# Performance work log

Measured on AMD Instinct MI355X. Metric: run time of the kernel, lower is better.

Reference implementation:

```python
import jax, jax.numpy as jnp
import numpy as np

B, C_IN, C_OUT, L = 16, 512, 512, 2048
HEADS, K, U, KS, PAD = 4, 16, 1, 3, 1
VV = C_OUT // HEADS  # 128
EPS = 1e-5


def _conv1d(x, w, pad):
    # x: [B, Cin, L], w: [Cout, Cin, KS] -> [B, Cout, L]
    return jax.lax.conv_general_dilated(
        x, w, window_strides=(1,), padding=[(pad, pad)],
        dimension_numbers=('NCH', 'OIH', 'NCH'))


def _bn_eval(y, gamma, beta, mean, var):
    # inference-mode BatchNorm1d over channel axis
    scale = gamma * jax.lax.rsqrt(var + EPS)
    shift = beta - mean * scale
    return y * scale[None, :, None] + shift[None, :, None]


def setup_inputs() -> dict:
    key = jax.random.key(0)
    ks = jax.random.split(key, 8)
    std_q = 1.0 / np.sqrt(C_IN * KS)
    x = jax.random.normal(ks[0], (B, C_IN, L), dtype=jnp.float32)
    Wq = jax.random.normal(ks[1], (K * HEADS, C_IN, KS), dtype=jnp.float32) * std_q
    Wk = jax.random.normal(ks[2], (K * U, C_IN, KS), dtype=jnp.float32) * std_q
    Wv = jax.random.normal(ks[3], (VV * U, C_IN, KS), dtype=jnp.float32) * std_q
    embedding = jax.random.normal(ks[4], (K, U), dtype=jnp.float32)
    return {
        'x': x, 'Wq': Wq,
        'q_gamma': jnp.ones((K * HEADS,), jnp.float32),
        'q_beta': jnp.zeros((K * HEADS,), jnp.float32),
        'q_mean': jnp.zeros((K * HEADS,), jnp.float32),
        'q_var': jnp.ones((K * HEADS,), jnp.float32),
        'Wk': Wk, 'Wv': Wv,
        'v_gamma': jnp.ones((VV * U,), jnp.float32),
        'v_beta': jnp.zeros((VV * U,), jnp.float32),
        'v_mean': jnp.zeros((VV * U,), jnp.float32),
        'v_var': jnp.ones((VV * U,), jnp.float32),
        'embedding': embedding,
    }


def reference(x, Wq, q_gamma, q_beta, q_mean, q_var, Wk, Wv,
              v_gamma, v_beta, v_mean, v_var, embedding):
    batch, _, n = x.shape
    # projections
    q = _bn_eval(_conv1d(x, Wq, PAD), q_gamma, q_beta, q_mean, q_var)
    q = q.reshape(batch, HEADS, K, n)                      # bhkn
    keys = _conv1d(x, Wk, PAD).reshape(batch, K, U, n)     # bkun
    sm = jax.nn.softmax(keys, axis=-1)                     # softmax over positions
    v = _bn_eval(_conv1d(x, Wv, PAD), v_gamma, v_beta, v_mean, v_var)
    v = v.reshape(batch, VV, U, n)                         # bvun
    # content lambda
    lambda_c = jnp.einsum('bkun,bvun->bkv', sm, v)
    y_c = jnp.einsum('bhkn,bkv->bhvn', q, lambda_c)
    # position lambda
    lambda_p = jnp.einsum('ku,bvun->bkvn', embedding, v)
    y_p = jnp.einsum('bhkn,bkvn->bhvn', q, lambda_p)
    out = y_c + y_p
    return out.reshape(batch, HEADS * VV, n)
```

## Files before the change

kernel.cpp:

```cpp
#include <hip/hip_runtime.h>

#define BB 16
#define CIN 512
#define LLN 2048
#define EPSV 1e-5f

typedef __attribute__((ext_vector_type(8))) short bf16x8s;
typedef __attribute__((ext_vector_type(4))) float f32x4;

__device__ __forceinline__ unsigned short f2bf(float f) {
    union { float f; unsigned int i; } c; c.f = f;
    unsigned int x = c.i;
    unsigned int lsb = (x >> 16) & 1;
    x += 0x7fff + lsb;
    return (unsigned short)(x >> 16);
}
__device__ __forceinline__ unsigned int pack2bf(float a, float b) {
    return (unsigned int)f2bf(a) | ((unsigned int)f2bf(b) << 16);
}

__device__ __forceinline__ void g2l16(const void* g, void* l) {
    typedef const __attribute__((address_space(1))) unsigned int GU;
    typedef __attribute__((address_space(3))) unsigned int LU;
    __builtin_amdgcn_global_load_lds((GU*)g, (LU*)l, 16, 0, 0);
}

#define WIMG_U16 6144

__global__ __launch_bounds__(256) void prep_all(
    const float* __restrict__ x,
    const float* __restrict__ Wq, const float* __restrict__ Wk,
    const float* __restrict__ Wv,
    unsigned short* __restrict__ xpk, unsigned short* __restrict__ Wpk)
{
    const int tid = threadIdx.x;
    if (blockIdx.z < 16) {
        const int nt = blockIdx.x;
        const int c  = blockIdx.y;
        const int b  = blockIdx.z;
        const int n = nt * 256 + tid;
        const int rp = n + 1;
        const float* xb = x + ((size_t)b * CIN + (size_t)c * 32) * LLN + n;
        unsigned int row[16];
#pragma unroll
        for (int p = 0; p < 16; p++)
            row[p] = pack2bf(xb[(size_t)(2 * p) * LLN], xb[(size_t)(2 * p + 1) * LLN]);
        unsigned short* dst = xpk + ((size_t)(b * 16 + c) * 2050 + rp) * 32;
        const int sig = (rp >> 1) & 3;
#pragma unroll
        for (int s = 0; s < 4; s++) {
            int g = (s ^ sig) * 4;
            *(uint4*)(dst + s * 8) = make_uint4(row[g], row[g + 1], row[g + 2], row[g + 3]);
        }
        if (nt == 0 && tid < 4)
            *(uint4*)(xpk + ((size_t)(b * 16 + c) * 2050) * 32 + tid * 8) = make_uint4(0, 0, 0, 0);
        if (nt == 7 && tid < 4)
            *(uint4*)(xpk + ((size_t)(b * 16 + c) * 2050 + 2049) * 32 + tid * 8) = make_uint4(0, 0, 0, 0);
    } else {
        const int wblk = blockIdx.y * 8 + blockIdx.x;
        const int img = wblk >> 1, half = wblk & 1;
        const int cot = img >> 4, chunk = img & 15;
        const int ci0 = chunk * 32;
        for (int i = half * 3072 + tid; i < half * 3072 + 3072; i += 256) {
            int t = i >> 11, r = i & 2047;
            int cf = r >> 9, lane = (r >> 3) & 63, e = i & 7;
            int lm = lane & 15, kq = lane >> 4;
            int cop = cot * 64 + cf * 16 + lm;
            int cig = ci0 + kq * 8 + e;
            float val = 0.f;
            if (cop < 64)        val = Wq[((size_t)cop * 512 + cig) * 3 + t];
            else if (cop < 80)   val = Wk[((size_t)(cop - 64) * 512 + cig) * 3 + t];
            else if (cop < 208)  val = Wv[((size_t)(cop - 80) * 512 + cig) * 3 + t];
            Wpk[(size_t)img * WIMG_U16 + i] = f2bf(val);
        }
    }
}

__global__ __launch_bounds__(256) void conv_mfma(
    const unsigned short* __restrict__ xpk, const unsigned short* __restrict__ Wpk,
    const float* __restrict__ qg, const float* __restrict__ qb,
    const float* __restrict__ qm, const float* __restrict__ qv,
    const float* __restrict__ vg, const float* __restrict__ vb,
    const float* __restrict__ vm, const float* __restrict__ vvar,
    float* __restrict__ qbuf, float* __restrict__ kbuf, float* __restrict__ vbuf)
{
    __shared__ __align__(16) unsigned short xT[2][258 * 32];
    __shared__ __align__(16) unsigned short wA[2][WIMG_U16];
    __shared__ float sscale[64], sshift[64];

    const int tid = threadIdx.x;
    const int wave = tid >> 6, lane = tid & 63;
    const int kq = lane >> 4, lm = lane & 15;
    const int n0 = blockIdx.x * 256;
    const int cot = blockIdx.y;
    const int b = blockIdx.z;

    const unsigned short* xpanel = xpk + ((size_t)b * 16 * 2050 + n0) * 32;
    const unsigned short* wbase  = Wpk + (size_t)cot * 16 * WIMG_U16;

#define STAGE(buf, chunk)                                                      \
    {                                                                          \
        const unsigned short* wsrc = wbase + (size_t)(chunk) * WIMG_U16;       \
        const unsigned short* xsrc = xpanel + (size_t)(chunk) * 2050 * 32;     \
        for (int i = tid; i < 768; i += 256)  g2l16(wsrc + i * 8, &wA[buf][i * 8]); \
        for (int i = tid; i < 1032; i += 256) g2l16(xsrc + i * 8, &xT[buf][i * 8]); \
    }

    STAGE(0, 0)

    if (tid < 64) {
        int cop = cot * 64 + tid;
        float sc = 1.f, sh = 0.f;
        if (cop < 64) {
            float g = qg[cop], be = qb[cop], m = qm[cop], va = qv[cop];
            sc = g * rsqrtf(va + EPSV); sh = be - m * sc;
        } else if (cop >= 80 && cop < 208) {
            int cc = cop - 80;
            float g = vg[cc], be = vb[cc], m = vm[cc], va = vvar[cc];
            sc = g * rsqrtf(va + EPSV); sh = be - m * sc;
        }
        sscale[tid] = sc; sshift[tid] = sh;
    }

    f32x4 acc[4][4];
#pragma unroll
    for (int i = 0; i < 4; i++)
#pragma unroll
        for (int j = 0; j < 4; j++) acc[i][j] = (f32x4){0.f, 0.f, 0.f, 0.f};

    asm volatile("s_waitcnt vmcnt(0)" ::: "memory");
    __syncthreads();

    for (int chunk = 0; chunk < 16; chunk++) {
        const int cur = chunk & 1;
        if (chunk < 15) STAGE(cur ^ 1, chunk + 1)

#pragma unroll
        for (int t = 0; t < 3; t++) {
            bf16x8s aF[4];
#pragma unroll
            for (int cf = 0; cf < 4; cf++)
                aF[cf] = *(const bf16x8s*)&wA[cur][((t * 4 + cf) * 64 + lane) * 8];
#pragma unroll
            for (int fn = 0; fn < 4; fn++) {
                int lr = wave * 64 + fn * 16 + lm + t;
                int grp = kq ^ ((lr >> 1) & 3);
                bf16x8s bF = *(const bf16x8s*)&xT[cur][lr * 32 + grp * 8];
#pragma unroll
                for (int cf = 0; cf < 4; cf++)
                    acc[cf][fn] = __builtin_amdgcn_mfma_f32_16x16x32_bf16(
                        aF[cf], bF, acc[cf][fn], 0, 0, 0);
            }
        }
        asm volatile("s_waitcnt vmcnt(0)" ::: "memory");
        __syncthreads();
    }
#undef STAGE

#pragma unroll
    for (int cf = 0; cf < 4; cf++) {
#pragma unroll
        for (int fn = 0; fn < 4; fn++) {
#pragma unroll
            for (int r = 0; r < 4; r++) {
                int col = cf * 16 + kq * 4 + r;
                int cop = cot * 64 + col;
                if (cop >= 208) continue;
                float val = acc[cf][fn][r] * sscale[col] + sshift[col];
                int nout = n0 + wave * 64 + fn * 16 + lm;
                if (cop < 64)
                    qbuf[((size_t)b * 64 + cop) * LLN + nout] = val;
                else if (cop < 80)
                    kbuf[((size_t)b * 16 + (cop - 64)) * LLN + nout] = val;
                else
                    vbuf[((size_t)b * 128 + (cop - 80)) * LLN + nout] = val;
            }
        }
    }
}

__global__ __launch_bounds__(256) void lambdac_kernel(
    const float* __restrict__ kb, const float* __restrict__ vbuf,
    float* __restrict__ lcb)
{
    const int wave = threadIdx.x >> 6;
    const int lane = threadIdx.x & 63;
    const int b = blockIdx.x >> 5;
    const int vg = blockIdx.x & 31;
    const float* ps = kb + ((size_t)b * 16 + wave * 4) * LLN;
    const float* pv = vbuf + ((size_t)b * 128 + vg * 4) * LLN;

    float m[4] = {-1e30f, -1e30f, -1e30f, -1e30f};
#pragma unroll
    for (int j = 0; j < 8; j++) {
        int n = (j * 64 + lane) * 4;
#pragma unroll
        for (int k = 0; k < 4; k++) {
            float4 s4 = *(const float4*)&ps[(size_t)k * LLN + n];
            m[k] = fmaxf(m[k], fmaxf(fmaxf(s4.x, s4.y), fmaxf(s4.z, s4.w)));
        }
    }
#pragma unroll
    for (int k = 0; k < 4; k++)
#pragma unroll
        for (int off = 32; off > 0; off >>= 1)
            m[k] = fmaxf(m[k], __shfl_xor(m[k], off, 64));

    float sum[4] = {0.f, 0.f, 0.f, 0.f};
    float acc[4][4];
#pragma unroll
    for (int k = 0; k < 4; k++)
#pragma unroll
        for (int v = 0; v < 4; v++) acc[k][v] = 0.f;
#pragma unroll
    for (int j = 0; j < 8; j++) {
        int n = (j * 64 + lane) * 4;
        float4 e4[4];
#pragma unroll
        for (int k = 0; k < 4; k++) {
            float4 s4 = *(const float4*)&ps[(size_t)k * LLN + n];
            e4[k].x = __expf(s4.x - m[k]);
            e4[k].y = __expf(s4.y - m[k]);
            e4[k].z = __expf(s4.z - m[k]);
            e4[k].w = __expf(s4.w - m[k]);
            sum[k] += e4[k].x + e4[k].y + e4[k].z + e4[k].w;
        }
#pragma unroll
        for (int v = 0; v < 4; v++) {
            float4 v4 = *(const float4*)&pv[(size_t)v * LLN + n];
#pragma unroll
            for (int k = 0; k < 4; k++)
                acc[k][v] += e4[k].x * v4.x + e4[k].y * v4.y
                           + e4[k].z * v4.z + e4[k].w * v4.w;
        }
    }
#pragma unroll
    for (int k = 0; k < 4; k++) {
#pragma unroll
        for (int off = 32; off > 0; off >>= 1)
            sum[k] += __shfl_xor(sum[k], off, 64);
#pragma unroll
        for (int v = 0; v < 4; v++)
#pragma unroll
            for (int off = 32; off > 0; off >>= 1)
                acc[k][v] += __shfl_xor(acc[k][v], off, 64);
    }
    if (lane == 0) {
#pragma unroll
        for (int k = 0; k < 4; k++) {
            float inv = 1.f / sum[k];
#pragma unroll
            for (int v = 0; v < 4; v++)
                lcb[((size_t)b * 16 + wave * 4 + k) * 128 + vg * 4 + v] = acc[k][v] * inv;
        }
    }
}

__global__ __launch_bounds__(256) void final_kernel(
    const float* __restrict__ qbuf, const float* __restrict__ vbuf,
    const float* __restrict__ lcb, const float* __restrict__ emb,
    float* __restrict__ out)
{
    __shared__ float lcsT[128][16];
    __shared__ float es[16];
    const int tid = threadIdx.x;
    const int h = tid >> 6, nl = tid & 63;
    const int n0 = blockIdx.x * 64;
    const int b = blockIdx.y;

    for (int i = tid; i < 2048; i += 256)
        lcsT[i >> 4][i & 15] = lcb[(size_t)b * 2048 + (size_t)(i & 15) * 128 + (i >> 4)];
    if (tid < 16) es[tid] = emb[tid];
    __syncthreads();

    const int n = n0 + nl;
    const float* pq = qbuf + ((size_t)b * 64 + h * 16) * LLN + n;
    float4 q4[4];
#pragma unroll
    for (int kk = 0; kk < 4; kk++) {
        q4[kk].x = pq[(size_t)(kk * 4 + 0) * LLN];
        q4[kk].y = pq[(size_t)(kk * 4 + 1) * LLN];
        q4[kk].z = pq[(size_t)(kk * 4 + 2) * LLN];
        q4[kk].w = pq[(size_t)(kk * 4 + 3) * LLN];
    }
    float s = 0.f;
#pragma unroll
    for (int kk = 0; kk < 4; kk++)
        s += q4[kk].x * es[kk * 4] + q4[kk].y * es[kk * 4 + 1]
           + q4[kk].z * es[kk * 4 + 2] + q4[kk].w * es[kk * 4 + 3];

    const float* pv = vbuf + (size_t)b * 128 * LLN + n;
    float* po = out + ((size_t)b * 512 + h * 128) * LLN + n;
    for (int v = 0; v < 128; v++) {
        float4 c0 = *(const float4*)&lcsT[v][0];
        float4 c1 = *(const float4*)&lcsT[v][4];
        float4 c2 = *(const float4*)&lcsT[v][8];
        float4 c3 = *(const float4*)&lcsT[v][12];
        float lam = q4[0].x * c0.x + q4[0].y * c0.y + q4[0].z * c0.z + q4[0].w * c0.w
                  + q4[1].x * c1.x + q4[1].y * c1.y + q4[1].z * c1.z + q4[1].w * c1.w
                  + q4[2].x * c2.x + q4[2].y * c2.y + q4[2].z * c2.z + q4[2].w * c2.w
                  + q4[3].x * c3.x + q4[3].y * c3.y + q4[3].z * c3.z + q4[3].w * c3.w;
        float vvv = pv[(size_t)v * LLN];
        po[(size_t)v * LLN] = lam + s * vvv;
    }
}

extern "C" void kernel_launch(void* const* d_in, const int* in_sizes, int n_in,
                              void* d_out, int out_size, void* d_ws, size_t ws_size,
                              hipStream_t stream)
{
    const float* x   = (const float*)d_in[0];
    const float* Wq  = (const float*)d_in[1];
    const float* qg  = (const float*)d_in[2];
    const float* qb  = (const float*)d_in[3];
    const float* qm  = (const float*)d_in[4];
    const float* qv  = (const float*)d_in[5];
    const float* Wk  = (const float*)d_in[6];
    const float* Wv  = (const float*)d_in[7];
    const float* vg  = (const float*)d_in[8];
    const float* vb  = (const float*)d_in[9];
    const float* vm  = (const float*)d_in[10];
    const float* vva = (const float*)d_in[11];
    const float* emb = (const float*)d_in[12];
    float* out = (float*)d_out;

    float* qbuf = (float*)d_ws;
    float* kbuf = qbuf + (size_t)BB * 64 * LLN;
    float* vbuf = kbuf + (size_t)BB * 16 * LLN;
    float* lcb  = vbuf + (size_t)BB * 128 * LLN;
    unsigned short* Wpk = (unsigned short*)(lcb + (size_t)BB * 16 * 128);
    unsigned short* xpk = Wpk + (size_t)64 * WIMG_U16;

    hipLaunchKernelGGL(prep_all, dim3(8, 16, 17), dim3(256), 0, stream,
                       x, Wq, Wk, Wv, xpk, Wpk);

    hipLaunchKernelGGL(conv_mfma, dim3(8, 4, 16), dim3(256), 0, stream,
                       xpk, Wpk, qg, qb, qm, qv, vg, vb, vm, vva,
                       qbuf, kbuf, vbuf);

    hipLaunchKernelGGL(lambdac_kernel, dim3(512), dim3(256), 0, stream,
                       kbuf, vbuf, lcb);

    hipLaunchKernelGGL(final_kernel, dim3(32, BB), dim3(256), 0, stream,
                       qbuf, vbuf, lcb, emb, out);
}
```

Baseline: 204.2 us.

## Store q and v intermediates as bf16 and vectorize x packing

The conv kernel now writes q and v projections as bf16 instead of fp32, and the lambda and final kernels read and widen them, halving intermediate memory traffic. The lambda kernel is reworked to process 8 positions per lane with 16-byte bf16 loads. The x prep kernel now has each thread load float4s and pack 4 positions, using 4x fewer blocks, and the weight prep gives each block two full images. This adds bf16 rounding error to q and v before the final products.

```diff
diff --git a/kernel.cpp b/kernel.cpp
--- a/kernel.cpp
+++ b/kernel.cpp
@@ -18,6 +18,15 @@
 __device__ __forceinline__ unsigned int pack2bf(float a, float b) {
     return (unsigned int)f2bf(a) | ((unsigned int)f2bf(b) << 16);
 }
+__device__ __forceinline__ float bf2f(unsigned short u) {
+    union { unsigned int i; float f; } c; c.i = ((unsigned int)u) << 16; return c.f;
+}
+__device__ __forceinline__ float bflo(unsigned int w) {
+    union { unsigned int i; float f; } c; c.i = w << 16; return c.f;
+}
+__device__ __forceinline__ float bfhi(unsigned int w) {
+    union { unsigned int i; float f; } c; c.i = w & 0xffff0000u; return c.f;
+}
 
 __device__ __forceinline__ void g2l16(const void* g, void* l) {
     typedef const __attribute__((address_space(1))) unsigned int GU;
@@ -38,40 +47,53 @@
         const int nt = blockIdx.x;
         const int c  = blockIdx.y;
         const int b  = blockIdx.z;
-        const int n = nt * 256 + tid;
-        const int rp = n + 1;
+        const int n = nt * 1024 + tid * 4;
         const float* xb = x + ((size_t)b * CIN + (size_t)c * 32) * LLN + n;
-        unsigned int row[16];
-#pragma unroll
-        for (int p = 0; p < 16; p++)
-            row[p] = pack2bf(xb[(size_t)(2 * p) * LLN], xb[(size_t)(2 * p + 1) * LLN]);
-        unsigned short* dst = xpk + ((size_t)(b * 16 + c) * 2050 + rp) * 32;
-        const int sig = (rp >> 1) & 3;
-#pragma unroll
-        for (int s = 0; s < 4; s++) {
-            int g = (s ^ sig) * 4;
-            *(uint4*)(dst + s * 8) = make_uint4(row[g], row[g + 1], row[g + 2], row[g + 3]);
+        unsigned short* dstbase = xpk + ((size_t)(b * 16 + c) * 2050 + (n + 1)) * 32;
+#pragma unroll
+        for (int g = 0; g < 4; g++) {
+            float4 r[8];
+#pragma unroll
+            for (int q = 0; q < 8; q++)
+                r[q] = *(const float4*)&xb[(size_t)(g * 8 + q) * LLN];
+#pragma unroll
+            for (int dn = 0; dn < 4; dn++) {
+                const float* rr[8] = {(const float*)&r[0], (const float*)&r[1],
+                                      (const float*)&r[2], (const float*)&r[3],
+                                      (const float*)&r[4], (const float*)&r[5],
+                                      (const float*)&r[6], (const float*)&r[7]};
+                uint4 w = make_uint4(pack2bf(rr[0][dn], rr[1][dn]),
+                                     pack2bf(rr[2][dn], rr[3][dn]),
+                                     pack2bf(rr[4][dn], rr[5][dn]),
+                                     pack2bf(rr[6][dn], rr[7][dn]));
+                int rp = n + dn + 1;
+                int sp = g ^ ((rp >> 1) & 3);
+                *(uint4*)(dstbase + (size_t)dn * 32 + sp * 8) = w;
+            }
         }
         if (nt == 0 && tid < 4)
             *(uint4*)(xpk + ((size_t)(b * 16 + c) * 2050) * 32 + tid * 8) = make_uint4(0, 0, 0, 0);
-        if (nt == 7 && tid < 4)
+        if (nt == 1 && tid < 4)
             *(uint4*)(xpk + ((size_t)(b * 16 + c) * 2050 + 2049) * 32 + tid * 8) = make_uint4(0, 0, 0, 0);
     } else {
-        const int wblk = blockIdx.y * 8 + blockIdx.x;
-        const int img = wblk >> 1, half = wblk & 1;
-        const int cot = img >> 4, chunk = img & 15;
-        const int ci0 = chunk * 32;
-        for (int i = half * 3072 + tid; i < half * 3072 + 3072; i += 256) {
-            int t = i >> 11, r = i & 2047;
-            int cf = r >> 9, lane = (r >> 3) & 63, e = i & 7;
-            int lm = lane & 15, kq = lane >> 4;
-            int cop = cot * 64 + cf * 16 + lm;
-            int cig = ci0 + kq * 8 + e;
-            float val = 0.f;
-            if (cop < 64)        val = Wq[((size_t)cop * 512 + cig) * 3 + t];
-            else if (cop < 80)   val = Wk[((size_t)(cop - 64) * 512 + cig) * 3 + t];
-            else if (cop < 208)  val = Wv[((size_t)(cop - 80) * 512 + cig) * 3 + t];
-            Wpk[(size_t)img * WIMG_U16 + i] = f2bf(val);
+        const int wblk = blockIdx.y * 2 + blockIdx.x;
+#pragma unroll
+        for (int which = 0; which < 2; which++) {
+            const int img = wblk * 2 + which;
+            const int cot = img >> 4, chunk = img & 15;
+            const int ci0 = chunk * 32;
+            for (int i = tid; i < WIMG_U16; i += 256) {
+                int t = i >> 11, r = i & 2047;
+                int cf = r >> 9, lane = (r >> 3) & 63, e = i & 7;
+                int lm = lane & 15, kq = lane >> 4;
+                int cop = cot * 64 + cf * 16 + lm;
+                int cig = ci0 + kq * 8 + e;
+                float val = 0.f;
+                if (cop < 64)        val = Wq[((size_t)cop * 512 + cig) * 3 + t];
+                else if (cop < 80)   val = Wk[((size_t)(cop - 64) * 512 + cig) * 3 + t];
+                else if (cop < 208)  val = Wv[((size_t)(cop - 80) * 512 + cig) * 3 + t];
+                Wpk[(size_t)img * WIMG_U16 + i] = f2bf(val);
+            }
         }
     }
 }
@@ -82,7 +104,8 @@
     const float* __restrict__ qm, const float* __restrict__ qv,
     const float* __restrict__ vg, const float* __restrict__ vb,
     const float* __restrict__ vm, const float* __restrict__ vvar,
-    float* __restrict__ qbuf, float* __restrict__ kbuf, float* __restrict__ vbuf)
+    unsigned short* __restrict__ qb16, float* __restrict__ kbuf,
+    unsigned short* __restrict__ vb16)
 {
     __shared__ __align__(16) unsigned short xT[2][258 * 32];
     __shared__ __align__(16) unsigned short wA[2][WIMG_U16];
@@ -169,18 +192,18 @@
                 float val = acc[cf][fn][r] * sscale[col] + sshift[col];
                 int nout = n0 + wave * 64 + fn * 16 + lm;
                 if (cop < 64)
-                    qbuf[((size_t)b * 64 + cop) * LLN + nout] = val;
+                    qb16[((size_t)b * 64 + cop) * LLN + nout] = f2bf(val);
                 else if (cop < 80)
                     kbuf[((size_t)b * 16 + (cop - 64)) * LLN + nout] = val;
                 else
-                    vbuf[((size_t)b * 128 + (cop - 80)) * LLN + nout] = val;
+                    vb16[((size_t)b * 128 + (cop - 80)) * LLN + nout] = f2bf(val);
             }
         }
     }
 }
 
 __global__ __launch_bounds__(256) void lambdac_kernel(
-    const float* __restrict__ kb, const float* __restrict__ vbuf,
+    const float* __restrict__ kb, const unsigned short* __restrict__ vb16,
     float* __restrict__ lcb)
 {
     const int wave = threadIdx.x >> 6;
@@ -188,16 +211,18 @@
     const int b = blockIdx.x >> 5;
     const int vg = blockIdx.x & 31;
     const float* ps = kb + ((size_t)b * 16 + wave * 4) * LLN;
-    const float* pv = vbuf + ((size_t)b * 128 + vg * 4) * LLN;
+    const unsigned short* pv = vb16 + ((size_t)b * 128 + vg * 4) * LLN;
 
     float m[4] = {-1e30f, -1e30f, -1e30f, -1e30f};
 #pragma unroll
-    for (int j = 0; j < 8; j++) {
-        int n = (j * 64 + lane) * 4;
+    for (int j = 0; j < 4; j++) {
+        int n = (j * 64 + lane) * 8;
 #pragma unroll
         for (int k = 0; k < 4; k++) {
-            float4 s4 = *(const float4*)&ps[(size_t)k * LLN + n];
-            m[k] = fmaxf(m[k], fmaxf(fmaxf(s4.x, s4.y), fmaxf(s4.z, s4.w)));
+            float4 a = *(const float4*)&ps[(size_t)k * LLN + n];
+            float4 c = *(const float4*)&ps[(size_t)k * LLN + n + 4];
+            m[k] = fmaxf(m[k], fmaxf(fmaxf(fmaxf(a.x, a.y), fmaxf(a.z, a.w)),
+                                     fmaxf(fmaxf(c.x, c.y), fmaxf(c.z, c.w))));
         }
     }
 #pragma unroll
@@ -213,25 +238,32 @@
 #pragma unroll
         for (int v = 0; v < 4; v++) acc[k][v] = 0.f;
 #pragma unroll
-    for (int j = 0; j < 8; j++) {
-        int n = (j * 64 + lane) * 4;
-        float4 e4[4];
+    for (int j = 0; j < 4; j++) {
+        int n = (j * 64 + lane) * 8;
+        float e[4][8];
 #pragma unroll
         for (int k = 0; k < 4; k++) {
-            float4 s4 = *(const float4*)&ps[(size_t)k * LLN + n];
-            e4[k].x = __expf(s4.x - m[k]);
-            e4[k].y = __expf(s4.y - m[k]);
-            e4[k].z = __expf(s4.z - m[k]);
-            e4[k].w = __expf(s4.w - m[k]);
-            sum[k] += e4[k].x + e4[k].y + e4[k].z + e4[k].w;
+            float4 a = *(const float4*)&ps[(size_t)k * LLN + n];
+            float4 c = *(const float4*)&ps[(size_t)k * LLN + n + 4];
+            e[k][0] = __expf(a.x - m[k]); e[k][1] = __expf(a.y - m[k]);
+            e[k][2] = __expf(a.z - m[k]); e[k][3] = __expf(a.w - m[k]);
+            e[k][4] = __expf(c.x - m[k]); e[k][5] = __expf(c.y - m[k]);
+            e[k][6] = __expf(c.z - m[k]); e[k][7] = __expf(c.w - m[k]);
+#pragma unroll
+            for (int q = 0; q < 8; q++) sum[k] += e[k][q];
         }
 #pragma unroll
         for (int v = 0; v < 4; v++) {
-            float4 v4 = *(const float4*)&pv[(size_t)v * LLN + n];
-#pragma unroll
-            for (int k = 0; k < 4; k++)
-                acc[k][v] += e4[k].x * v4.x + e4[k].y * v4.y
-                           + e4[k].z * v4.z + e4[k].w * v4.w;
+            uint4 w = *(const uint4*)&pv[(size_t)v * LLN + n];
+            float vv[8] = {bflo(w.x), bfhi(w.x), bflo(w.y), bfhi(w.y),
+                           bflo(w.z), bfhi(w.z), bflo(w.w), bfhi(w.w)};
+#pragma unroll
+            for (int k = 0; k < 4; k++) {
+                float t = 0.f;
+#pragma unroll
+                for (int q = 0; q < 8; q++) t += e[k][q] * vv[q];
+                acc[k][v] += t;
+            }
         }
     }
 #pragma unroll
@@ -257,7 +289,7 @@
 }
 
 __global__ __launch_bounds__(256) void final_kernel(
-    const float* __restrict__ qbuf, const float* __restrict__ vbuf,
+    const unsigned short* __restrict__ qb16, const unsigned short* __restrict__ vb16,
     const float* __restrict__ lcb, const float* __restrict__ emb,
     float* __restrict__ out)
 {
@@ -274,14 +306,14 @@
     __syncthreads();
 
     const int n = n0 + nl;
-    const float* pq = qbuf + ((size_t)b * 64 + h * 16) * LLN + n;
+    const unsigned short* pq = qb16 + ((size_t)b * 64 + h * 16) * LLN + n;
     float4 q4[4];
 #pragma unroll
     for (int kk = 0; kk < 4; kk++) {
-        q4[kk].x = pq[(size_t)(kk * 4 + 0) * LLN];
-        q4[kk].y = pq[(size_t)(kk * 4 + 1) * LLN];
-        q4[kk].z = pq[(size_t)(kk * 4 + 2) * LLN];
-        q4[kk].w = pq[(size_t)(kk * 4 + 3) * LLN];
+        q4[kk].x = bf2f(pq[(size_t)(kk * 4 + 0) * LLN]);
+        q4[kk].y = bf2f(pq[(size_t)(kk * 4 + 1) * LLN]);
+        q4[kk].z = bf2f(pq[(size_t)(kk * 4 + 2) * LLN]);
+        q4[kk].w = bf2f(pq[(size_t)(kk * 4 + 3) * LLN]);
     }
     float s = 0.f;
 #pragma unroll
@@ -289,7 +321,7 @@
         s += q4[kk].x * es[kk * 4] + q4[kk].y * es[kk * 4 + 1]
            + q4[kk].z * es[kk * 4 + 2] + q4[kk].w * es[kk * 4 + 3];
 
-    const float* pv = vbuf + (size_t)b * 128 * LLN + n;
+    const unsigned short* pv = vb16 + (size_t)b * 128 * LLN + n;
     float* po = out + ((size_t)b * 512 + h * 128) * LLN + n;
     for (int v = 0; v < 128; v++) {
         float4 c0 = *(const float4*)&lcsT[v][0];
@@ -300,7 +332,7 @@
                   + q4[1].x * c1.x + q4[1].y * c1.y + q4[1].z * c1.z + q4[1].w * c1.w
                   + q4[2].x * c2.x + q4[2].y * c2.y + q4[2].z * c2.z + q4[2].w * c2.w
                   + q4[3].x * c3.x + q4[3].y * c3.y + q4[3].z * c3.z + q4[3].w * c3.w;
-        float vvv = pv[(size_t)v * LLN];
+        float vvv = bf2f(pv[(size_t)v * LLN]);
         po[(size_t)v * LLN] = lam + s * vvv;
     }
 }
@@ -324,23 +356,23 @@
     const float* emb = (const float*)d_in[12];
     float* out = (float*)d_out;
 
-    float* qbuf = (float*)d_ws;
-    float* kbuf = qbuf + (size_t)BB * 64 * LLN;
-    float* vbuf = kbuf + (size_t)BB * 16 * LLN;
-    float* lcb  = vbuf + (size_t)BB * 128 * LLN;
-    unsigned short* Wpk = (unsigned short*)(lcb + (size_t)BB * 16 * 128);
-    unsigned short* xpk = Wpk + (size_t)64 * WIMG_U16;
-
-    hipLaunchKernelGGL(prep_all, dim3(8, 16, 17), dim3(256), 0, stream,
+    float* kbuf = (float*)d_ws;
+    float* lcb  = kbuf + (size_t)BB * 16 * LLN;
+    unsigned short* qb16 = (unsigned short*)(lcb + (size_t)BB * 16 * 128);
+    unsigned short* vb16 = qb16 + (size_t)BB * 64 * LLN;
+    unsigned short* Wpk  = vb16 + (size_t)BB * 128 * LLN;
+    unsigned short* xpk  = Wpk + (size_t)64 * WIMG_U16;
+
+    hipLaunchKernelGGL(prep_all, dim3(2, 16, 17), dim3(256), 0, stream,
                        x, Wq, Wk, Wv, xpk, Wpk);
 
     hipLaunchKernelGGL(conv_mfma, dim3(8, 4, 16), dim3(256), 0, stream,
                        xpk, Wpk, qg, qb, qm, qv, vg, vb, vm, vva,
-                       qbuf, kbuf, vbuf);
+                       qb16, kbuf, vb16);
 
     hipLaunchKernelGGL(lambdac_kernel, dim3(512), dim3(256), 0, stream,
-                       kbuf, vbuf, lcb);
+                       kbuf, vb16, lcb);
 
     hipLaunchKernelGGL(final_kernel, dim3(32, BB), dim3(256), 0, stream,
-                       qbuf, vbuf, lcb, emb, out);
-}
+                       qb16, vb16, lcb, emb, out);
+}
```

Measured after the change: 227.9 us. 11.6% more time.
